# Performance work log

Hardware: AMD Instinct MI355X
Metric: run time of the kernel (lower is better)

The kernel has to match this reference:

```python
import jax, jax.numpy as jnp
import numpy as np

BS, DIM = 8192, 768
TEMPERATURE = 1.0
EPS = 1e-8


def setup_inputs() -> dict:
    key = jax.random.key(0)
    k1, k2 = jax.random.split(key)
    text_emb = jax.random.normal(k1, (BS, DIM), dtype=jnp.float32)
    ctr_emb = jax.random.normal(k2, (BS, DIM), dtype=jnp.float32)
    return {"text_emb": text_emb, "ctr_emb": ctr_emb}


def _l2norm(x):
    # cosine scorer normalization
    return x / jnp.maximum(jnp.linalg.norm(x, axis=-1, keepdims=True), EPS)


def reference(text_emb, ctr_emb):
    t = _l2norm(text_emb)          # [bs, d]
    c = _l2norm(ctr_emb)           # [bs, d]
    # S[i, j] = cos(text_i, ctr_j) / T  -- single GEMM instead of (bs,bs,d) broadcast
    S = jnp.einsum('id,jd->ij', t, c) / TEMPERATURE   # [bs, bs]
    sim_ii = jnp.diagonal(S)                           # [bs]
    # loss1_i = lse_j S[i,j] - S[i,i]; loss2_i = lse_j S[j,i] - S[i,i]
    loss = (jax.nn.logsumexp(S, axis=1)
            + jax.nn.logsumexp(S, axis=0)
            - 2.0 * sim_ii)
    return jnp.mean(loss)
```

## Files before the change

### kernel.cpp

```cpp
#include <hip/hip_runtime.h>
#include <hip/hip_bf16.h>

#define BS   8192
#define DIM  768
#define BM   256
#define BK   128

typedef float f32x4 __attribute__((ext_vector_type(4)));
typedef int   i32x4 __attribute__((ext_vector_type(4)));
typedef int   i32x8 __attribute__((ext_vector_type(8)));

__device__ __forceinline__ void async16(const void* g, void* l) {
    __builtin_amdgcn_global_load_lds(
        (const __attribute__((address_space(1))) unsigned int*)g,
        (__attribute__((address_space(3))) unsigned int*)l,
        16, 0, 0);
}

__global__ __launch_bounds__(256) void normalize_kernel(
    const float* __restrict__ text, const float* __restrict__ ctr,
    unsigned char* __restrict__ tq, unsigned char* __restrict__ cq,
    float* __restrict__ sim, float* __restrict__ rowsum, float* __restrict__ colsum) {
    if (blockIdx.x < 64) {
        const int i = blockIdx.x * 256 + threadIdx.x;
        rowsum[i] = 0.f;
        colsum[i] = 0.f;
    }
    const int lane = threadIdx.x & 63;
    const int row  = blockIdx.x * 4 + (threadIdx.x >> 6);
    const size_t base = (size_t)row * DIM;

    float4 t[3], c[3];
    float st = 0.f, sc = 0.f, sd = 0.f;
#pragma unroll
    for (int i = 0; i < 3; ++i) {
        t[i] = *(const float4*)&text[base + lane * 4 + i * 256];
        c[i] = *(const float4*)&ctr [base + lane * 4 + i * 256];
        st += t[i].x*t[i].x + t[i].y*t[i].y + t[i].z*t[i].z + t[i].w*t[i].w;
        sc += c[i].x*c[i].x + c[i].y*c[i].y + c[i].z*c[i].z + c[i].w*c[i].w;
        sd += t[i].x*c[i].x + t[i].y*c[i].y + t[i].z*c[i].z + t[i].w*c[i].w;
    }
#pragma unroll
    for (int off = 1; off < 64; off <<= 1) {
        st += __shfl_xor(st, off);
        sc += __shfl_xor(sc, off);
        sd += __shfl_xor(sd, off);
    }
    const float invt = 1.0f / fmaxf(sqrtf(st), 1e-8f);
    const float invc = 1.0f / fmaxf(sqrtf(sc), 1e-8f);
#pragma unroll
    for (int i = 0; i < 3; ++i) {
        unsigned int wt = (unsigned int)__builtin_amdgcn_cvt_pk_fp8_f32(t[i].x * invt, t[i].y * invt, 0, false);
        wt = (unsigned int)__builtin_amdgcn_cvt_pk_fp8_f32(t[i].z * invt, t[i].w * invt, (int)wt, true);
        unsigned int wcq = (unsigned int)__builtin_amdgcn_cvt_pk_fp8_f32(c[i].x * invc, c[i].y * invc, 0, false);
        wcq = (unsigned int)__builtin_amdgcn_cvt_pk_fp8_f32(c[i].z * invc, c[i].w * invc, (int)wcq, true);
        *(unsigned int*)&tq[base + lane * 4 + i * 256] = wt;
        *(unsigned int*)&cq[base + lane * 4 + i * 256] = wcq;
    }
    if (lane == 0) sim[row] = sd * invt * invc;
}

__global__ __launch_bounds__(512, 2) void gemm_lse_kernel(
    const unsigned char* __restrict__ tq, const unsigned char* __restrict__ cq,
    float* __restrict__ rowsum, float* __restrict__ colsum) {
    __shared__ char ldsA[2][BM * BK];
    __shared__ char ldsB[2][BM * BK];

    const int tid = threadIdx.x;

    const int bid = blockIdx.x;
    const int xcd = bid & 7, idx = bid >> 3;
    const int tileCol = idx >> 2, rowInBand = idx & 3;
    const int rowBase = (xcd * 4 + rowInBand) * BM;
    const int colBase = tileCol * BM;

    const int wave = tid >> 6, lane = tid & 63;
    const int wr = wave >> 2, wc = wave & 3;
    const int quad = lane >> 4, l16 = lane & 15;

    int goff[4], p16[4];
#pragma unroll
    for (int i = 0; i < 4; ++i) {
        const int p  = tid + i * 512;
        const int kc = p >> 9;
        const int row = (p >> 1) & 255;
        const int hl  = (p & 1) ^ (kc & 1);
        goff[i] = row * DIM + kc * 32 + hl * 16;
        p16[i]  = p * 16;
    }
    const unsigned char* gA = tq + (size_t)rowBase * DIM;
    const unsigned char* gB = cq + (size_t)colBase * DIM;

#define STAGE(buf, t, i)                                            \
    do {                                                            \
        async16(gA + goff[i] + (t) * BK, &ldsA[buf][p16[i]]);       \
        async16(gB + goff[i] + (t) * BK, &ldsB[buf][p16[i]]);       \
    } while (0)

    const int sw = quad & 1;
    int aoff[8], boff[4];
#pragma unroll
    for (int mt = 0; mt < 8; ++mt) aoff[mt] = quad * 8192 + (wr * 128 + mt * 16 + l16) * 32;
#pragma unroll
    for (int nt = 0; nt < 4; ++nt) boff[nt] = quad * 8192 + (wc * 64 + nt * 16 + l16) * 32;

#define RD_A(dst, mt, buf)                                                     \
    do {                                                                       \
        i32x4 lo = *(const i32x4*)(ldsA[buf] + aoff[mt] + sw * 16);            \
        i32x4 hi = *(const i32x4*)(ldsA[buf] + aoff[mt] + (sw ^ 1) * 16);      \
        dst = __builtin_shufflevector(lo, hi, 0, 1, 2, 3, 4, 5, 6, 7);         \
    } while (0)
#define RD_B(dst, nt, buf)                                                     \
    do {                                                                       \
        i32x4 lo = *(const i32x4*)(ldsB[buf] + boff[nt] + sw * 16);            \
        i32x4 hi = *(const i32x4*)(ldsB[buf] + boff[nt] + (sw ^ 1) * 16);      \
        dst = __builtin_shufflevector(lo, hi, 0, 1, 2, 3, 4, 5, 6, 7);         \
    } while (0)
#define MFMA8(a0, a1, m0, m1)                                                  \
    do {                                                                       \
        acc[m0][0] = __builtin_amdgcn_mfma_scale_f32_16x16x128_f8f6f4(a0, bf0, acc[m0][0], 0, 0, 0, 127, 0, 127); \
        acc[m0][1] = __builtin_amdgcn_mfma_scale_f32_16x16x128_f8f6f4(a0, bf1, acc[m0][1], 0, 0, 0, 127, 0, 127); \
        acc[m0][2] = __builtin_amdgcn_mfma_scale_f32_16x16x128_f8f6f4(a0, bf2, acc[m0][2], 0, 0, 0, 127, 0, 127); \
        acc[m0][3] = __builtin_amdgcn_mfma_scale_f32_16x16x128_f8f6f4(a0, bf3, acc[m0][3], 0, 0, 0, 127, 0, 127); \
        acc[m1][0] = __builtin_amdgcn_mfma_scale_f32_16x16x128_f8f6f4(a1, bf0, acc[m1][0], 0, 0, 0, 127, 0, 127); \
        acc[m1][1] = __builtin_amdgcn_mfma_scale_f32_16x16x128_f8f6f4(a1, bf1, acc[m1][1], 0, 0, 0, 127, 0, 127); \
        acc[m1][2] = __builtin_amdgcn_mfma_scale_f32_16x16x128_f8f6f4(a1, bf2, acc[m1][2], 0, 0, 0, 127, 0, 127); \
        acc[m1][3] = __builtin_amdgcn_mfma_scale_f32_16x16x128_f8f6f4(a1, bf3, acc[m1][3], 0, 0, 0, 127, 0, 127); \
    } while (0)
#define SBAR()  __builtin_amdgcn_sched_barrier(0)

    f32x4 acc[8][4];
#pragma unroll
    for (int mt = 0; mt < 8; ++mt)
#pragma unroll
        for (int nt = 0; nt < 4; ++nt)
            acc[mt][nt] = (f32x4){0.f, 0.f, 0.f, 0.f};

    STAGE(0, 0, 0); STAGE(0, 0, 1); STAGE(0, 0, 2); STAGE(0, 0, 3);
    SBAR();
    STAGE(1, 1, 0);
    SBAR();
    asm volatile("s_waitcnt vmcnt(2)" ::: "memory");
    SBAR();
    __builtin_amdgcn_s_barrier();

#pragma unroll
    for (int t = 0; t < 6; ++t) {
        const int cur = t & 1;
        i32x8 bf0, bf1, bf2, bf3, aE0, aE1, aO0, aO1;

        RD_B(bf0, 0, cur); RD_B(bf1, 1, cur); RD_B(bf2, 2, cur); RD_B(bf3, 3, cur);
        RD_A(aE0, 0, cur); RD_A(aE1, 1, cur);

        RD_A(aO0, 2, cur); RD_A(aO1, 3, cur);
        if (t < 5) STAGE(cur ^ 1, t + 1, 1);
        asm volatile("s_waitcnt lgkmcnt(4)" ::: "memory");
        SBAR();
        __builtin_amdgcn_s_setprio(1);
        MFMA8(aE0, aE1, 0, 1);
        __builtin_amdgcn_s_setprio(0);

        RD_A(aE0, 4, cur); RD_A(aE1, 5, cur);
        if (t < 5) STAGE(cur ^ 1, t + 1, 2);
        asm volatile("s_waitcnt lgkmcnt(4)" ::: "memory");
        SBAR();
        __builtin_amdgcn_s_setprio(1);
        MFMA8(aO0, aO1, 2, 3);
        __builtin_amdgcn_s_setprio(0);

        RD_A(aO0, 6, cur); RD_A(aO1, 7, cur);
        if (t < 5) STAGE(cur ^ 1, t + 1, 3);
        asm volatile("s_waitcnt lgkmcnt(4)" ::: "memory");
        SBAR();
        __builtin_amdgcn_s_setprio(1);
        MFMA8(aE0, aE1, 4, 5);
        __builtin_amdgcn_s_setprio(0);

        asm volatile("s_waitcnt lgkmcnt(0)" ::: "memory");
        SBAR();
        __builtin_amdgcn_s_setprio(1);
        MFMA8(aO0, aO1, 6, 7);
        __builtin_amdgcn_s_setprio(0);

        if (t < 5) {
            __builtin_amdgcn_s_barrier();
            SBAR();
            if (t < 4) {
                STAGE(cur, t + 2, 0);
                SBAR();
                asm volatile("s_waitcnt vmcnt(2)" ::: "memory");
            } else {
                asm volatile("s_waitcnt vmcnt(0)" ::: "memory");
            }
            SBAR();
            __builtin_amdgcn_s_barrier();
        }
    }

    float rp[8][4];
    float cp[4];
#pragma unroll
    for (int mt = 0; mt < 8; ++mt)
#pragma unroll
        for (int r = 0; r < 4; ++r) rp[mt][r] = 0.f;
#pragma unroll
    for (int nt = 0; nt < 4; ++nt) cp[nt] = 0.f;

#pragma unroll
    for (int mt = 0; mt < 8; ++mt)
#pragma unroll
        for (int nt = 0; nt < 4; ++nt)
#pragma unroll
            for (int r = 0; r < 4; ++r) {
                const float e = __expf(acc[mt][nt][r]);
                rp[mt][r] += e;
                cp[nt]    += e;
            }

#pragma unroll
    for (int mt = 0; mt < 8; ++mt)
#pragma unroll
        for (int r = 0; r < 4; ++r) {
            float v = rp[mt][r];
            v += __shfl_xor(v, 1);
            v += __shfl_xor(v, 2);
            v += __shfl_xor(v, 4);
            v += __shfl_xor(v, 8);
            rp[mt][r] = v;
        }
    if (l16 == 0) {
#pragma unroll
        for (int mt = 0; mt < 8; ++mt)
#pragma unroll
            for (int r = 0; r < 4; ++r)
                atomicAdd(&rowsum[rowBase + wr * 128 + mt * 16 + quad * 4 + r], rp[mt][r]);
    }
#pragma unroll
    for (int nt = 0; nt < 4; ++nt) {
        float v = cp[nt];
        v += __shfl_xor(v, 16);
        v += __shfl_xor(v, 32);
        if (quad == 0)
            atomicAdd(&colsum[colBase + wc * 64 + nt * 16 + l16], v);
    }
}

__global__ __launch_bounds__(1024) void finalize_kernel(
    const float* __restrict__ rowsum, const float* __restrict__ colsum,
    const float* __restrict__ sim, float* __restrict__ out) {
    const int tid = threadIdx.x;
    float acc = 0.f;
#pragma unroll
    for (int i = 0; i < 2; ++i) {
        const int j = (tid + i * 1024) * 4;
        float4 rs = *(const float4*)&rowsum[j];
        float4 cs = *(const float4*)&colsum[j];
        float4 sm = *(const float4*)&sim[j];
        acc += __logf(rs.x) + __logf(rs.y) + __logf(rs.z) + __logf(rs.w);
        acc += __logf(cs.x) + __logf(cs.y) + __logf(cs.z) + __logf(cs.w);
        acc -= 2.f * (sm.x + sm.y + sm.z + sm.w);
    }
#pragma unroll
    for (int off = 1; off < 64; off <<= 1) acc += __shfl_xor(acc, off);
    __shared__ float red[16];
    const int wave = tid >> 6, lane = tid & 63;
    if (lane == 0) red[wave] = acc;
    __syncthreads();
    if (tid == 0) {
        float s = 0.f;
#pragma unroll
        for (int w = 0; w < 16; ++w) s += red[w];
        out[0] = s / (float)BS;
    }
}

extern "C" void kernel_launch(void* const* d_in, const int* in_sizes, int n_in,
                              void* d_out, int out_size, void* d_ws, size_t ws_size,
                              hipStream_t stream) {
    const float* text = (const float*)d_in[0];
    const float* ctr  = (const float*)d_in[1];

    char* ws = (char*)d_ws;
    const size_t embBytes = (size_t)BS * DIM;
    unsigned char* tq = (unsigned char*)ws;
    unsigned char* cq = (unsigned char*)(ws + embBytes);
    float* sim    = (float*)(ws + 2 * embBytes);
    float* rowsum = (float*)(ws + 2 * embBytes + BS * sizeof(float));
    float* colsum = (float*)(ws + 2 * embBytes + 2 * BS * sizeof(float));

    normalize_kernel<<<BS / 4, 256, 0, stream>>>(text, ctr, tq, cq, sim, rowsum, colsum);

    gemm_lse_kernel<<<(BS / BM) * (BS / BM), 512, 0, stream>>>(tq, cq, rowsum, colsum);

    finalize_kernel<<<1, 1024, 0, stream>>>(rowsum, colsum, sim, (float*)d_out);
}
```

Measured before the change: 169.9 us.

## Fuse finalize into GEMM via last-block ticket and restructure barrier schedule

Removes the separate finalize kernel launch. The GEMM blocks now increment a global ticket counter, and the last block to finish computes the log-sum reduction and writes the output. The main loop also gains extra workgroup barriers around each MFMA phase, and the next-stage prefetch is moved ahead of the final MFMA group to overlap loads with compute. The added barriers may cost some wave interleaving. The last-block reduction serializes a small tail onto one block.

```diff
diff --git a/kernel.cpp b/kernel.cpp
--- a/kernel.cpp
+++ b/kernel.cpp
@@ -5,6 +5,7 @@
 #define DIM  768
 #define BM   256
 #define BK   128
+#define NBLK ((BS / BM) * (BS / BM))
 
 typedef float f32x4 __attribute__((ext_vector_type(4)));
 typedef int   i32x4 __attribute__((ext_vector_type(4)));
@@ -20,12 +21,14 @@
 __global__ __launch_bounds__(256) void normalize_kernel(
     const float* __restrict__ text, const float* __restrict__ ctr,
     unsigned char* __restrict__ tq, unsigned char* __restrict__ cq,
-    float* __restrict__ sim, float* __restrict__ rowsum, float* __restrict__ colsum) {
+    float* __restrict__ sim, float* __restrict__ rowsum, float* __restrict__ colsum,
+    unsigned int* __restrict__ cnt) {
     if (blockIdx.x < 64) {
         const int i = blockIdx.x * 256 + threadIdx.x;
         rowsum[i] = 0.f;
         colsum[i] = 0.f;
     }
+    if (blockIdx.x == 0 && threadIdx.x == 0) cnt[0] = 0u;
     const int lane = threadIdx.x & 63;
     const int row  = blockIdx.x * 4 + (threadIdx.x >> 6);
     const size_t base = (size_t)row * DIM;
@@ -62,7 +65,9 @@
 
 __global__ __launch_bounds__(512, 2) void gemm_lse_kernel(
     const unsigned char* __restrict__ tq, const unsigned char* __restrict__ cq,
-    float* __restrict__ rowsum, float* __restrict__ colsum) {
+    float* __restrict__ rowsum, float* __restrict__ colsum,
+    const float* __restrict__ sim, unsigned int* __restrict__ cnt,
+    float* __restrict__ out) {
     __shared__ char ldsA[2][BM * BK];
     __shared__ char ldsB[2][BM * BK];
 
@@ -154,44 +159,46 @@
 
         RD_A(aO0, 2, cur); RD_A(aO1, 3, cur);
         if (t < 5) STAGE(cur ^ 1, t + 1, 1);
+        __builtin_amdgcn_s_barrier();
         asm volatile("s_waitcnt lgkmcnt(4)" ::: "memory");
         SBAR();
         __builtin_amdgcn_s_setprio(1);
         MFMA8(aE0, aE1, 0, 1);
         __builtin_amdgcn_s_setprio(0);
+        __builtin_amdgcn_s_barrier();
 
         RD_A(aE0, 4, cur); RD_A(aE1, 5, cur);
         if (t < 5) STAGE(cur ^ 1, t + 1, 2);
+        __builtin_amdgcn_s_barrier();
         asm volatile("s_waitcnt lgkmcnt(4)" ::: "memory");
         SBAR();
         __builtin_amdgcn_s_setprio(1);
         MFMA8(aO0, aO1, 2, 3);
         __builtin_amdgcn_s_setprio(0);
+        __builtin_amdgcn_s_barrier();
 
         RD_A(aO0, 6, cur); RD_A(aO1, 7, cur);
         if (t < 5) STAGE(cur ^ 1, t + 1, 3);
+        __builtin_amdgcn_s_barrier();
         asm volatile("s_waitcnt lgkmcnt(4)" ::: "memory");
         SBAR();
         __builtin_amdgcn_s_setprio(1);
         MFMA8(aE0, aE1, 4, 5);
         __builtin_amdgcn_s_setprio(0);
+        __builtin_amdgcn_s_barrier();
 
         asm volatile("s_waitcnt lgkmcnt(0)" ::: "memory");
         SBAR();
+        if (t < 5) {
+            __builtin_amdgcn_s_barrier();
+            if (t < 4) STAGE(cur, t + 2, 0);
+        }
         __builtin_amdgcn_s_setprio(1);
         MFMA8(aO0, aO1, 6, 7);
         __builtin_amdgcn_s_setprio(0);
-
         if (t < 5) {
-            __builtin_amdgcn_s_barrier();
-            SBAR();
-            if (t < 4) {
-                STAGE(cur, t + 2, 0);
-                SBAR();
-                asm volatile("s_waitcnt vmcnt(2)" ::: "memory");
-            } else {
-                asm volatile("s_waitcnt vmcnt(0)" ::: "memory");
-            }
+            if (t < 4) asm volatile("s_waitcnt vmcnt(2)" ::: "memory");
+            else       asm volatile("s_waitcnt vmcnt(0)" ::: "memory");
             SBAR();
             __builtin_amdgcn_s_barrier();
         }
@@ -243,34 +250,34 @@
         if (quad == 0)
             atomicAdd(&colsum[colBase + wc * 64 + nt * 16 + l16], v);
     }
-}
-
-__global__ __launch_bounds__(1024) void finalize_kernel(
-    const float* __restrict__ rowsum, const float* __restrict__ colsum,
-    const float* __restrict__ sim, float* __restrict__ out) {
-    const int tid = threadIdx.x;
-    float acc = 0.f;
-#pragma unroll
-    for (int i = 0; i < 2; ++i) {
-        const int j = (tid + i * 1024) * 4;
-        float4 rs = *(const float4*)&rowsum[j];
-        float4 cs = *(const float4*)&colsum[j];
-        float4 sm = *(const float4*)&sim[j];
-        acc += __logf(rs.x) + __logf(rs.y) + __logf(rs.z) + __logf(rs.w);
-        acc += __logf(cs.x) + __logf(cs.y) + __logf(cs.z) + __logf(cs.w);
-        acc -= 2.f * (sm.x + sm.y + sm.z + sm.w);
-    }
-#pragma unroll
-    for (int off = 1; off < 64; off <<= 1) acc += __shfl_xor(acc, off);
-    __shared__ float red[16];
-    const int wave = tid >> 6, lane = tid & 63;
-    if (lane == 0) red[wave] = acc;
+
+    unsigned int* tick = (unsigned int*)&ldsA[0][0];
     __syncthreads();
     if (tid == 0) {
-        float s = 0.f;
-#pragma unroll
-        for (int w = 0; w < 16; ++w) s += red[w];
-        out[0] = s / (float)BS;
+        __threadfence();
+        tick[0] = __hip_atomic_fetch_add(cnt, 1u, __ATOMIC_ACQ_REL, __HIP_MEMORY_SCOPE_AGENT);
+    }
+    __syncthreads();
+    if (tick[0] == NBLK - 1) {
+        float a2 = 0.f;
+#pragma unroll
+        for (int k = 0; k < 16; ++k) {
+            const int i = tid + k * 512;
+            const float rs = __hip_atomic_load(&rowsum[i], __ATOMIC_RELAXED, __HIP_MEMORY_SCOPE_AGENT);
+            const float cs = __hip_atomic_load(&colsum[i], __ATOMIC_RELAXED, __HIP_MEMORY_SCOPE_AGENT);
+            a2 += __logf(rs) + __logf(cs) - 2.f * sim[i];
+        }
+#pragma unroll
+        for (int off = 1; off < 64; off <<= 1) a2 += __shfl_xor(a2, off);
+        float* red = (float*)&ldsB[0][0];
+        if (lane == 0) red[wave] = a2;
+        __syncthreads();
+        if (tid == 0) {
+            float s = 0.f;
+#pragma unroll
+            for (int w = 0; w < 8; ++w) s += red[w];
+            out[0] = s / (float)BS;
+        }
     }
 }
 
@@ -287,10 +294,9 @@
     float* sim    = (float*)(ws + 2 * embBytes);
     float* rowsum = (float*)(ws + 2 * embBytes + BS * sizeof(float));
     float* colsum = (float*)(ws + 2 * embBytes + 2 * BS * sizeof(float));
-
-    normalize_kernel<<<BS / 4, 256, 0, stream>>>(text, ctr, tq, cq, sim, rowsum, colsum);
-
-    gemm_lse_kernel<<<(BS / BM) * (BS / BM), 512, 0, stream>>>(tq, cq, rowsum, colsum);
-
-    finalize_kernel<<<1, 1024, 0, stream>>>(rowsum, colsum, sim, (float*)d_out);
+    unsigned int* cnt = (unsigned int*)(ws + 2 * embBytes + 3 * BS * sizeof(float));
+
+    normalize_kernel<<<BS / 4, 256, 0, stream>>>(text, ctr, tq, cq, sim, rowsum, colsum, cnt);
+
+    gemm_lse_kernel<<<NBLK, 512, 0, stream>>>(tq, cq, rowsum, colsum, sim, cnt, (float*)d_out);
 }
```

Measured after the change: 200.7 us. 1.18x slower.
